# Performance work log

Measured on AMD Instinct MI355X. Metric: run time of the kernel, lower is better.

Reference implementation:

```python
import jax, jax.numpy as jnp
import numpy as np

NUM_ITEMS = 1000000   # catalog size; id == NUM_ITEMS is the padding item
B, S = 512, 200       # batch, sequence length
M, SUB = 8, 32        # pq_m bytes per item, sub-embedding size (embedding_size = M*SUB = 256)
NUM_CENTROIDS = 256   # uint8 code range


def setup_inputs() -> dict:
    key = jax.random.key(0)
    k1, k2, k3 = jax.random.split(key, 3)
    input_ids = jax.random.randint(k1, (B, S), 0, NUM_ITEMS + 1, dtype=jnp.int64)
    # item_codes: PQ code table, one byte (0..255) per item per code-byte
    item_codes = jax.random.randint(k2, (NUM_ITEMS + 1, M), 0, NUM_CENTROIDS, dtype=jnp.int32)
    # centroids: per-byte codebooks, uniform init as in tf.random_uniform_initializer()
    centroids = jax.random.uniform(k3, (M, NUM_CENTROIDS, SUB), dtype=jnp.float32)
    return {"input_ids": input_ids, "item_codes": item_codes, "centroids": centroids}


def reference(input_ids, item_codes, centroids):
    # codes[b,s,i] = PQ byte i of item input_ids[b,s]
    codes = item_codes[input_ids]                                  # [B, S, M] int32
    byte_idx = jnp.arange(codes.shape[-1])[None, None, :]          # [1, 1, M]
    # gather centroid vector per (byte, code): centroids[i, codes[b,s,i], :]
    sub_emb = centroids[byte_idx, codes]                           # [B, S, M, SUB]
    b, s = input_ids.shape
    return sub_emb.reshape(b, s, codes.shape[-1] * centroids.shape[-1])  # [B, S, M*SUB]
```

## Files before the change

kernel.cpp:

```cpp
#include <hip/hip_runtime.h>


typedef float f4 __attribute__((ext_vector_type(4)));

#define M_BYTES 8
#define SUB_DIM 32
#define EMB     (M_BYTES * SUB_DIM)
#define TPW     8
#define WAVES   4
#define TOK_PER_BLOCK (TPW * WAVES)
#define BLOCK   256

__global__ __launch_bounds__(BLOCK) void ItemCodeLayer_30253749633338_kernel(
    const int*   __restrict__ ids,
    const int*   __restrict__ codes,
    const float* __restrict__ cent,
    float*       __restrict__ out,
    int n_tokens)
{
    const int tid  = threadIdx.x;
    const int l    = tid & 63;
    const int wave = __builtin_amdgcn_readfirstlane(tid >> 6);
    const int lm   = l >> 3;
    const int l4   = l * 4;

    const float* centBase = cent + (size_t)lm * 256 * SUB_DIM + (l & 7) * 4;

    const int t0 = blockIdx.x * TOK_PER_BLOCK + wave * TPW;

    if (t0 + TPW <= n_tokens) {
        int c[TPW];
        #pragma unroll
        for (int k = 0; k < TPW; ++k) {
            int id = ids[t0 + k];
            c[k] = __builtin_nontemporal_load(codes + (size_t)id * M_BYTES + lm);
        }
        f4 v[TPW];
        #pragma unroll
        for (int k = 0; k < TPW; ++k)
            v[k] = *reinterpret_cast<const f4*>(centBase + (size_t)c[k] * SUB_DIM);
        #pragma unroll
        for (int k = 0; k < TPW; ++k)
            *reinterpret_cast<f4*>(out + (size_t)(t0 + k) * EMB + l4) = v[k];
    } else if (t0 < n_tokens) {
        #pragma unroll
        for (int k = 0; k < TPW; ++k) {
            int t = t0 + k;
            if (t < n_tokens) {
                int id  = ids[t];
                int cd  = codes[(size_t)id * M_BYTES + lm];
                f4 val  = *reinterpret_cast<const f4*>(centBase + (size_t)cd * SUB_DIM);
                *reinterpret_cast<f4*>(out + (size_t)t * EMB + l4) = val;
            }
        }
    }
}

extern "C" void kernel_launch(void* const* d_in, const int* in_sizes, int n_in,
                              void* d_out, int out_size, void* d_ws, size_t ws_size,
                              hipStream_t stream) {
    const int*   ids   = (const int*)  d_in[0];
    const int*   codes = (const int*)  d_in[1];
    const float* cent  = (const float*)d_in[2];
    float*       out   = (float*)      d_out;

    const int n_tokens = in_sizes[0];
    const int grid = (n_tokens + TOK_PER_BLOCK - 1) / TOK_PER_BLOCK;

    hipLaunchKernelGGL(ItemCodeLayer_30253749633338_kernel,
                       dim3(grid), dim3(BLOCK), 0, stream,
                       ids, codes, cent, out, n_tokens);
}
```

Baseline: 133.4 us.

## Use persistent grid-stride waves with software-pipelined code prefetch

Turns the one-chunk-per-wave launch into a persistent grid of up to 1024 blocks, where each wave walks chunks with a grid stride. While the current chunk's centroid loads are in flight, it prefetches the next chunk's ids and codes, so the dependent ids->codes->centroids gather latency overlaps with stores. The trade-off is fewer waves in flight for latency hiding, extra registers for the prefetch buffers, and clamped tail indices.

```diff
diff --git a/kernel.cpp b/kernel.cpp
--- a/kernel.cpp
+++ b/kernel.cpp
@@ -8,8 +8,8 @@
 #define EMB     (M_BYTES * SUB_DIM)
 #define TPW     8
 #define WAVES   4
-#define TOK_PER_BLOCK (TPW * WAVES)
 #define BLOCK   256
+#define GRID_BLOCKS 1024
 
 __global__ __launch_bounds__(BLOCK) void ItemCodeLayer_30253749633338_kernel(
     const int*   __restrict__ ids,
@@ -20,39 +20,64 @@
 {
     const int tid  = threadIdx.x;
     const int l    = tid & 63;
-    const int wave = __builtin_amdgcn_readfirstlane(tid >> 6);
+    const int wave = tid >> 6;
     const int lm   = l >> 3;
     const int l4   = l * 4;
 
     const float* centBase = cent + (size_t)lm * 256 * SUB_DIM + (l & 7) * 4;
 
-    const int t0 = blockIdx.x * TOK_PER_BLOCK + wave * TPW;
+    const int nchunks = (n_tokens + TPW - 1) / TPW;
+    const int stride  = gridDim.x * WAVES;
+    int chunk = blockIdx.x * WAVES + wave;
+    if (chunk >= nchunks) return;
 
-    if (t0 + TPW <= n_tokens) {
-        int c[TPW];
+    const int last = n_tokens - 1;
+
+    int c[TPW];
+    {
+        const int t0 = chunk * TPW;
         #pragma unroll
         for (int k = 0; k < TPW; ++k) {
-            int id = ids[t0 + k];
+            int t = t0 + k; if (t > last) t = last;
+            int id = ids[t];
             c[k] = __builtin_nontemporal_load(codes + (size_t)id * M_BYTES + lm);
         }
+    }
+
+    for (;;) {
+        const int t0   = chunk * TPW;
+        const int next = chunk + stride;
+        const bool have_next = next < nchunks;
+
         f4 v[TPW];
         #pragma unroll
         for (int k = 0; k < TPW; ++k)
             v[k] = *reinterpret_cast<const f4*>(centBase + (size_t)c[k] * SUB_DIM);
-        #pragma unroll
-        for (int k = 0; k < TPW; ++k)
-            *reinterpret_cast<f4*>(out + (size_t)(t0 + k) * EMB + l4) = v[k];
-    } else if (t0 < n_tokens) {
+
+        __builtin_amdgcn_sched_barrier(0);
+
+        int cn[TPW];
+        if (have_next) {
+            const int tn = next * TPW;
+            #pragma unroll
+            for (int k = 0; k < TPW; ++k) {
+                int t = tn + k; if (t > last) t = last;
+                int id = ids[t];
+                cn[k] = __builtin_nontemporal_load(codes + (size_t)id * M_BYTES + lm);
+            }
+        }
+
         #pragma unroll
         for (int k = 0; k < TPW; ++k) {
             int t = t0 + k;
-            if (t < n_tokens) {
-                int id  = ids[t];
-                int cd  = codes[(size_t)id * M_BYTES + lm];
-                f4 val  = *reinterpret_cast<const f4*>(centBase + (size_t)cd * SUB_DIM);
-                *reinterpret_cast<f4*>(out + (size_t)t * EMB + l4) = val;
-            }
+            if (t < n_tokens)
+                *reinterpret_cast<f4*>(out + (size_t)t * EMB + l4) = v[k];
         }
+
+        if (!have_next) break;
+        chunk = next;
+        #pragma unroll
+        for (int k = 0; k < TPW; ++k) c[k] = cn[k];
     }
 }
 
@@ -65,7 +90,9 @@
     float*       out   = (float*)      d_out;
 
     const int n_tokens = in_sizes[0];
-    const int grid = (n_tokens + TOK_PER_BLOCK - 1) / TOK_PER_BLOCK;
+    const int nchunks  = (n_tokens + TPW - 1) / TPW;
+    int grid = (nchunks + WAVES - 1) / WAVES;
+    if (grid > GRID_BLOCKS) grid = GRID_BLOCKS;
 
     hipLaunchKernelGGL(ItemCodeLayer_30253749633338_kernel,
                        dim3(grid), dim3(BLOCK), 0, stream,
```

Result: slower. 137.4 us (+3.0%).
